# Kernel optimization log

Hardware: AMD Instinct MI355X
Metric: run time of the kernel (lower is better)

Reference implementation:

```python
import jax, jax.numpy as jnp
import numpy as np

D_MODEL = 512
NUM_HEADS = 8
DEPTH = D_MODEL // NUM_HEADS


def setup_inputs() -> dict:
    key = jax.random.key(0)
    ks = jax.random.split(key, 9)
    B, S = 2, 2048
    x = jax.random.normal(ks[0], (B, S, D_MODEL), dtype=jnp.float32)
    s = 1.0 / np.sqrt(D_MODEL)
    Wq = jax.random.uniform(ks[1], (D_MODEL, D_MODEL), minval=-s, maxval=s)
    bq = jax.random.uniform(ks[2], (D_MODEL,), minval=-s, maxval=s)
    Wk = jax.random.uniform(ks[3], (D_MODEL, D_MODEL), minval=-s, maxval=s)
    bk = jax.random.uniform(ks[4], (D_MODEL,), minval=-s, maxval=s)
    Wv = jax.random.uniform(ks[5], (D_MODEL, D_MODEL), minval=-s, maxval=s)
    bv = jax.random.uniform(ks[6], (D_MODEL,), minval=-s, maxval=s)
    Wo = jax.random.uniform(ks[7], (D_MODEL, D_MODEL), minval=-s, maxval=s)
    bo = jax.random.uniform(ks[8], (D_MODEL,), minval=-s, maxval=s)
    return {"x": x, "Wq": Wq, "bq": bq, "Wk": Wk, "bk": bk,
            "Wv": Wv, "bv": bv, "Wo": Wo, "bo": bo}


def _split_heads(t, B, S):
    # [B,S,D] -> [B,H,S,depth]
    return t.reshape(B, S, NUM_HEADS, DEPTH).transpose(0, 2, 1, 3)


def reference(x, Wq, bq, Wk, bk, Wv, bv, Wo, bo):
    B, S, _ = x.shape
    q = _split_heads(x @ Wq.T + bq, B, S) / jnp.sqrt(jnp.float32(DEPTH))
    k = _split_heads(x @ Wk.T + bk, B, S)
    v = _split_heads(x @ Wv.T + bv, B, S)
    scores = jnp.einsum('bhsd,bhtd->bhst', q, k)  # [B,H,S,S]
    attn = jax.nn.softmax(scores, axis=-1)
    out = jnp.einsum('bhst,bhtd->bhsd', attn, v)  # [B,H,S,depth]
    out = out.transpose(0, 2, 1, 3).reshape(B, S, D_MODEL)
    return out @ Wo.T + bo
```

## Files before the change

kernel.cpp:

```cpp
#include <hip/hip_runtime.h>

typedef unsigned int   uint32;
typedef unsigned short ushort16;

constexpr int BATCH = 2;
constexpr int SEQ   = 2048;
constexpr int DM    = 512;
constexpr int NH    = 8;
constexpr int DP    = 64;
constexpr int MROWS = BATCH * SEQ;
constexpr size_t HEADS_ELEMS = (size_t)BATCH * NH * SEQ * DP;

typedef short bf16x8 __attribute__((ext_vector_type(8)));
typedef float f32x4  __attribute__((ext_vector_type(4)));
typedef float f32x16 __attribute__((ext_vector_type(16)));
#define MFMA16(a, b, c) __builtin_amdgcn_mfma_f32_16x16x32_bf16((a), (b), (c), 0, 0, 0)
#define MFMA32(a, b, c) __builtin_amdgcn_mfma_f32_32x32x16_bf16((a), (b), (c), 0, 0, 0)

__device__ __forceinline__ ushort16 f2bf(float f) {
    uint32 u = __float_as_uint(f);
    uint32 r = (u + 0x7fffu + ((u >> 16) & 1u)) >> 16;
    return (ushort16)r;
}

__device__ __forceinline__ uint32 cvtpk(float a, float b) {
    uint32 r;
    asm("v_cvt_pk_bf16_f32 %0, %1, %2" : "=v"(r) : "v"(a), "v"(b));
    return r;
}

__device__ __forceinline__ bf16x8 mkfrag(uint32 u0, uint32 u1, uint32 u2, uint32 u3) {
    union { uint32 u[4]; bf16x8 v; } t;
    t.u[0] = u0; t.u[1] = u1; t.u[2] = u2; t.u[3] = u3;
    return t.v;
}

__device__ __forceinline__ void gload16(const void* g, void* l) {
    __builtin_amdgcn_global_load_lds(
        (const __attribute__((address_space(1))) unsigned int*)g,
        (__attribute__((address_space(3))) unsigned int*)l, 16, 0, 0);
}

constexpr int XF4 = (MROWS * DM) / 4;
constexpr int WF4 = (DM * DM) / 4;

__global__ __launch_bounds__(256)
void convert_inputs(const float4* __restrict__ x,  const float4* __restrict__ wq,
                    const float4* __restrict__ wk, const float4* __restrict__ wv,
                    const float4* __restrict__ wo, ushort4* __restrict__ xb,
                    ushort4* __restrict__ wqkv, ushort4* __restrict__ wob) {
    const int idx = blockIdx.x * 256 + threadIdx.x;
    float4 v; ushort4* dp;
    if (idx < XF4) { v = x[idx]; dp = xb + idx; }
    else {
        const int r = idx - XF4;
        if (r < WF4)          { v = wq[r];           dp = wqkv + r; }
        else if (r < 2 * WF4) { v = wk[r - WF4];     dp = wqkv + r; }
        else if (r < 3 * WF4) { v = wv[r - 2 * WF4]; dp = wqkv + r; }
        else                  { v = wo[r - 3 * WF4]; dp = wob + (r - 3 * WF4); }
    }
    ushort4 o = {f2bf(v.x), f2bf(v.y), f2bf(v.z), f2bf(v.w)};
    *dp = o;
}

template <int BM, int BN, int EPI, int NBX, int NBLK>
__global__ __launch_bounds__(256)
void gemm_mfma(const ushort16* __restrict__ X, const ushort16* __restrict__ Wc,
               const float* __restrict__ bq_, const float* __restrict__ bk_,
               const float* __restrict__ bv_, const float* __restrict__ bo_,
               ushort16* __restrict__ Qh, ushort16* __restrict__ Kh,
               ushort16* __restrict__ Vt, float* __restrict__ Out,
               float qscale) {
    constexpr int FM = BM / 32;
    constexpr int FN = BN / 32;
    __shared__ ushort16 As[BM * 64];
    __shared__ ushort16 Bs[BN * 64];

    const int tid  = threadIdx.x;
    const int lane = tid & 63;
    const int wid  = tid >> 6;
    const int lg   = lane >> 4;
    const int lq   = lane & 15;
    const int wr   = wid >> 1;
    const int wc   = wid & 1;

    const int bid = blockIdx.x;
    const int w   = (bid & 7) * (NBLK / 8) + (bid >> 3);
    const int bx  = w % NBX;
    const int by  = w / NBX;
    const int m0  = by * BM;
    const int n0  = bx * BN;
    const bool swapped = (EPI == 1) || (n0 < 2 * DM);

    f32x4 acc[FM][FN];
    #pragma unroll
    for (int i = 0; i < FM; i++)
        #pragma unroll
        for (int j = 0; j < FN; j++)
            #pragma unroll
            for (int r = 0; r < 4; r++) acc[i][j][r] = 0.f;

    for (int k0 = 0; k0 < DM; k0 += 64) {
        #pragma unroll
        for (int i = 0; i < BM / 32; i++) {
            const int ch = tid + i * 256;
            const int row = ch >> 3, c8 = (ch & 7) * 8;
            gload16(X + (size_t)(m0 + row) * DM + k0 + c8, As + (size_t)ch * 8);
        }
        #pragma unroll
        for (int i = 0; i < BN / 32; i++) {
            const int ch = tid + i * 256;
            const int row = ch >> 3, c8 = (ch & 7) * 8;
            gload16(Wc + (size_t)(n0 + row) * DM + k0 + c8, Bs + (size_t)ch * 8);
        }
        __syncthreads();

        bf16x8 af[FM][2], bfr[FN][2];
        #pragma unroll
        for (int i = 0; i < FM; i++)
            #pragma unroll
            for (int kk = 0; kk < 2; kk++)
                af[i][kk] = *(const bf16x8*)(As + (size_t)(wr * (BM / 2) + i * 16 + lq) * 64 + kk * 32 + lg * 8);
        #pragma unroll
        for (int j = 0; j < FN; j++)
            #pragma unroll
            for (int kk = 0; kk < 2; kk++)
                bfr[j][kk] = *(const bf16x8*)(Bs + (size_t)(wc * (BN / 2) + j * 16 + lq) * 64 + kk * 32 + lg * 8);

        if (swapped) {
            #pragma unroll
            for (int kk = 0; kk < 2; kk++)
                #pragma unroll
                for (int i = 0; i < FM; i++)
                    #pragma unroll
                    for (int j = 0; j < FN; j++)
                        acc[i][j] = MFMA16(bfr[j][kk], af[i][kk], acc[i][j]);
        } else {
            #pragma unroll
            for (int kk = 0; kk < 2; kk++)
                #pragma unroll
                for (int i = 0; i < FM; i++)
                    #pragma unroll
                    for (int j = 0; j < FN; j++)
                        acc[i][j] = MFMA16(af[i][kk], bfr[j][kk], acc[i][j]);
        }
        __syncthreads();
    }

    if (EPI == 1) {
        #pragma unroll
        for (int i = 0; i < FM; i++) {
            const int m = m0 + wr * (BM / 2) + i * 16 + lq;
            #pragma unroll
            for (int j = 0; j < FN; j++) {
                const int nr = n0 + wc * (BN / 2) + j * 16 + lg * 4;
                float4 b4 = *(const float4*)(bo_ + nr);
                float4 o;
                o.x = acc[i][j][0] + b4.x; o.y = acc[i][j][1] + b4.y;
                o.z = acc[i][j][2] + b4.z; o.w = acc[i][j][3] + b4.w;
                *(float4*)(Out + (size_t)m * DM + nr) = o;
            }
        }
    } else if (n0 < 2 * DM) {
        #pragma unroll
        for (int i = 0; i < FM; i++) {
            const int m = m0 + wr * (BM / 2) + i * 16 + lq;
            const int b = m >> 11, s = m & (SEQ - 1);
            #pragma unroll
            for (int j = 0; j < FN; j++) {
                const int nr = n0 + wc * (BN / 2) + j * 16 + lg * 4;
                const bool isq = nr < DM;
                const int rel = nr & (DM - 1);
                const int h = rel >> 6, d = rel & 63;
                float4 b4 = *(const float4*)((isq ? bq_ : bk_) + rel);
                const float sc = isq ? qscale : 1.0f;
                ushort4 o = { f2bf((acc[i][j][0] + b4.x) * sc),
                              f2bf((acc[i][j][1] + b4.y) * sc),
                              f2bf((acc[i][j][2] + b4.z) * sc),
                              f2bf((acc[i][j][3] + b4.w) * sc) };
                ushort16* dst = (isq ? Qh : Kh) +
                    (((size_t)(b * NH + h) * SEQ + s) * DP + d);
                *(ushort4*)dst = o;
            }
        }
    } else {
        #pragma unroll
        for (int j = 0; j < FN; j++) {
            const int n = n0 + wc * (BN / 2) + j * 16 + lq;
            const int rel = n - 2 * DM;
            const int h = rel >> 6, d = rel & 63;
            const float bias = bv_[rel];
            #pragma unroll
            for (int i = 0; i < FM; i++) {
                const int mr = m0 + wr * (BM / 2) + i * 16 + lg * 4;
                const int b = mr >> 11, s0 = mr & (SEQ - 1);
                ushort4 o = { f2bf(acc[i][j][0] + bias),
                              f2bf(acc[i][j][1] + bias),
                              f2bf(acc[i][j][2] + bias),
                              f2bf(acc[i][j][3] + bias) };
                ushort16* dst = Vt +
                    (((size_t)(b * NH + h) * DP + d) * SEQ + s0);
                *(ushort4*)dst = o;
            }
        }
    }
}

__global__ __launch_bounds__(1024, 1)
void attn_mfma(const ushort16* __restrict__ Q, const ushort16* __restrict__ K,
               const ushort16* __restrict__ Vt, ushort16* __restrict__ O) {
    __shared__ ushort16 Kl[3][128 * 64];
    __shared__ ushort16 Vl[3][64 * 128];
    __shared__ float    lbuf[4][4][32];

    const int tid  = threadIdx.x;
    const int lane = tid & 63;
    const int wid  = tid >> 6;
    const int qw   = wid & 3;
    const int kw   = wid >> 2;
    const int h    = lane >> 5;
    const int l31  = lane & 31;
    const int l7   = l31 & 7;

    const int bid = blockIdx.x;
    const int w   = (bid & 7) * 32 + (bid >> 3);
    const int qt  = w & 15;
    const int bh  = w >> 4;

    const int qrow = qt * 128 + qw * 32 + l31;
    const ushort16* qbase = Q + ((size_t)bh * SEQ + qrow) * DP;
    bf16x8 qf[4];
    #pragma unroll
    for (int ds = 0; ds < 4; ds++)
        qf[ds] = *(const bf16x8*)(qbase + ds * 16 + h * 8);

    f32x16 ok0, ok1;
    #pragma unroll
    for (int r = 0; r < 16; r++) { ok0[r] = 0.f; ok1[r] = 0.f; }
    float lrun = 0.f;

    const ushort16* kg = K  + (size_t)bh * SEQ * DP;
    const ushort16* vg = Vt + (size_t)bh * DP * SEQ;
    const int kr = tid >> 3, kc = tid & 7;
    const int ksrc = (kc ^ (kr & 7)) * 8;
    const ushort16* const kgp = kg + (size_t)kr * DP + ksrc;
    const int vr = tid >> 4, vc = tid & 15;
    const int vsrc = (vc ^ (vr & 7)) * 8;
    const ushort16* const vgp = vg + (size_t)vr * SEQ + vsrc;

    auto stage = [&](int buf, int t) {
        gload16(kgp + (size_t)t * 128 * DP, &Kl[buf][(size_t)tid * 8]);
        gload16(vgp + (size_t)t * 128,      &Vl[buf][(size_t)tid * 8]);
    };

    const int krow = kw * 32 + l31;
    int koff[4];
    #pragma unroll
    for (int ds = 0; ds < 4; ds++)
        koff[ds] = krow * 64 + (((ds * 2 + h) ^ l7) * 8);
    int voff[2][2];
    #pragma unroll
    for (int dt = 0; dt < 2; dt++)
        #pragma unroll
        for (int kc2 = 0; kc2 < 2; kc2++)
            voff[dt][kc2] = (dt * 32 + l31) * 128 + (((kw * 4 + kc2 * 2 + h) ^ l7) * 8);

    auto compute = [&](int buf) {
        const ushort16* kb = &Kl[buf][0];
        const ushort16* vb = &Vl[buf][0];
        f32x16 st;
        #pragma unroll
        for (int r = 0; r < 16; r++) st[r] = 0.f;
        __builtin_amdgcn_s_setprio(1);
        #pragma unroll
        for (int ds = 0; ds < 4; ds++) {
            bf16x8 kf = *(const bf16x8*)(kb + koff[ds]);
            st = MFMA32(kf, qf[ds], st);
        }
        __builtin_amdgcn_s_setprio(0);

        #pragma unroll
        for (int r = 0; r < 16; r++) {
            st[r] = __builtin_exp2f(st[r]);
            lrun += st[r];
        }

        uint32 A0 = cvtpk(st[0], st[1]),   A1 = cvtpk(st[2], st[3]);
        uint32 B0 = cvtpk(st[4], st[5]),   B1 = cvtpk(st[6], st[7]);
        uint32 C0 = cvtpk(st[8], st[9]),   C1 = cvtpk(st[10], st[11]);
        uint32 D0 = cvtpk(st[12], st[13]), D1 = cvtpk(st[14], st[15]);
        uint32 z0 = __shfl_xor((int)(h ? A0 : B0), 32);
        uint32 z1 = __shfl_xor((int)(h ? A1 : B1), 32);
        uint32 z2 = __shfl_xor((int)(h ? C0 : D0), 32);
        uint32 z3 = __shfl_xor((int)(h ? C1 : D1), 32);
        bf16x8 pa0 = h ? mkfrag(z0, z1, B0, B1) : mkfrag(A0, A1, z0, z1);
        bf16x8 pa1 = h ? mkfrag(z2, z3, D0, D1) : mkfrag(C0, C1, z2, z3);

        const bf16x8 v00 = *(const bf16x8*)(vb + voff[0][0]);
        const bf16x8 v01 = *(const bf16x8*)(vb + voff[0][1]);
        const bf16x8 v10 = *(const bf16x8*)(vb + voff[1][0]);
        const bf16x8 v11 = *(const bf16x8*)(vb + voff[1][1]);
        __builtin_amdgcn_s_setprio(1);
        ok0 = MFMA32(pa0, v00, ok0);
        ok0 = MFMA32(pa1, v01, ok0);
        ok1 = MFMA32(pa0, v10, ok1);
        ok1 = MFMA32(pa1, v11, ok1);
        __builtin_amdgcn_s_setprio(0);
    };

    #define WAITN(n) asm volatile("s_waitcnt vmcnt(" #n ")" ::: "memory")
    #define BAR() __builtin_amdgcn_s_barrier()

    stage(0, 0);
    stage(1, 1);
    int t = 0;
    #pragma unroll 1
    for (int it = 0; it < 4; ++it) {
        WAITN(2); BAR(); stage(2, t + 2); compute(0);
        WAITN(2); BAR(); stage(0, t + 3); compute(1);
        WAITN(2); BAR(); stage(1, t + 4); compute(2);
        t += 3;
    }
    WAITN(2); BAR(); stage(2, 14); compute(0);
    WAITN(2); BAR(); stage(0, 15); compute(1);
    WAITN(2); BAR(); compute(2);
    WAITN(0); BAR(); compute(0);
    #undef WAITN
    #undef BAR

    lrun += __shfl_xor(lrun, 32);

    __syncthreads();
    float* const fK = (float*)&Kl[0][0];
    float* const fV = (float*)&Vl[0][0];
    if (h == 0) lbuf[qw][kw][l31] = lrun;
    if (kw > 0) {
        const int ridx = (kw - 1) * 4 + qw;
        float* const dst = (ridx < 6) ? (fK + ridx * 2048) : (fV + (ridx - 6) * 2048);
        #pragma unroll
        for (int r = 0; r < 16; r++) {
            const int q = (r & 3) + 8 * (r >> 2) + 4 * h;
            dst[q * 64 + l31]      = ok0[r];
            dst[q * 64 + 32 + l31] = ok1[r];
        }
    }
    __syncthreads();
    if (kw == 0) {
        float* const p1 = fK + qw * 2048;
        float* const p2 = (qw < 2) ? (fK + (4 + qw) * 2048)
                                   : (fV + (qw - 2) * 2048);
        float* const p3 = fV + (2 + qw) * 2048;
        const float lsum = lbuf[qw][0][l31] + lbuf[qw][1][l31]
                         + lbuf[qw][2][l31] + lbuf[qw][3][l31];
        const float linv = 1.f / lsum;
        const int b = bh >> 3, hh = bh & 7;
        #pragma unroll
        for (int r = 0; r < 16; r++) {
            const int q = (r & 3) + 8 * (r >> 2) + 4 * h;
            const float li_q = __shfl(linv, q);
            const int o0 = q * 64 + l31;
            const int o1 = q * 64 + 32 + l31;
            const float v0 = (ok0[r] + p1[o0] + p2[o0] + p3[o0]) * li_q;
            const float v1 = (ok1[r] + p1[o1] + p2[o1] + p3[o1]) * li_q;
            const int qr = qt * 128 + qw * 32 + q;
            ushort16* orow = O + ((size_t)(b * SEQ + qr)) * DM + hh * DP;
            orow[l31]      = f2bf(v0);
            orow[32 + l31] = f2bf(v1);
        }
    }
}

extern "C" void kernel_launch(void* const* d_in, const int* in_sizes, int n_in,
                              void* d_out, int out_size, void* d_ws, size_t ws_size,
                              hipStream_t stream) {
    const float* x  = (const float*)d_in[0];
    const float* Wq = (const float*)d_in[1];
    const float* bq = (const float*)d_in[2];
    const float* Wk = (const float*)d_in[3];
    const float* bk = (const float*)d_in[4];
    const float* Wv = (const float*)d_in[5];
    const float* bv = (const float*)d_in[6];
    const float* Wo = (const float*)d_in[7];
    const float* bo = (const float*)d_in[8];
    float* out = (float*)d_out;

    ushort16* ws   = (ushort16*)d_ws;
    ushort16* xb   = ws;
    ushort16* wqkv = xb + (size_t)MROWS * DM;
    ushort16* wob  = wqkv + (size_t)3 * DM * DM;
    ushort16* qh   = wob + (size_t)DM * DM;
    ushort16* kh   = qh + HEADS_ELEMS;
    ushort16* vt   = kh + HEADS_ELEMS;
    ushort16* oh   = vt + HEADS_ELEMS;

    convert_inputs<<<dim3((XF4 + 4 * WF4) / 256), dim3(256), 0, stream>>>(
        (const float4*)x, (const float4*)Wq, (const float4*)Wk,
        (const float4*)Wv, (const float4*)Wo,
        (ushort4*)xb, (ushort4*)wqkv, (ushort4*)wob);

    const float qscale = 0.125f * 1.44269504088896f;

    gemm_mfma<128, 64, 0, 24, 768><<<dim3(768), dim3(256), 0, stream>>>(
        xb, wqkv, bq, bk, bv, bo, qh, kh, vt, nullptr, qscale);

    attn_mfma<<<dim3(256), dim3(1024), 0, stream>>>(qh, kh, vt, oh);

    gemm_mfma<64, 64, 1, 8, 512><<<dim3(512), dim3(256), 0, stream>>>(
        oh, wob, bq, bk, bv, bo, qh, kh, vt, out, qscale);
}
```

Before: 66.03 us.

## Fuse fp32-to-bf16 conversion of x into QKV GEMM and split QK accumulators

The separate pass that converts x to bf16 is removed. The QKV projection GEMM now reads fp32 x directly, packs it to bf16 with v_cvt_pk_bf16_f32 and writes it into shared memory. This saves a full write and re-read of the activation buffer but gives up async global_load_lds for the A tile, and x is now re-read once per N-tile (24 times). In the attention kernel the K and V LDS loads are hoisted to the top and the QK^T MFMA chain is split into two independent accumulators to shorten the dependency chain, at the cost of more registers.

Result: slower. 136.9 us (+107.3%).

```diff
diff --git a/kernel.cpp b/kernel.cpp
--- a/kernel.cpp
+++ b/kernel.cpp
@@ -41,31 +41,25 @@
         (__attribute__((address_space(3))) unsigned int*)l, 16, 0, 0);
 }
 
-constexpr int XF4 = (MROWS * DM) / 4;
 constexpr int WF4 = (DM * DM) / 4;
 
 __global__ __launch_bounds__(256)
-void convert_inputs(const float4* __restrict__ x,  const float4* __restrict__ wq,
-                    const float4* __restrict__ wk, const float4* __restrict__ wv,
-                    const float4* __restrict__ wo, ushort4* __restrict__ xb,
-                    ushort4* __restrict__ wqkv, ushort4* __restrict__ wob) {
-    const int idx = blockIdx.x * 256 + threadIdx.x;
+void convert_w(const float4* __restrict__ wq, const float4* __restrict__ wk,
+               const float4* __restrict__ wv, const float4* __restrict__ wo,
+               ushort4* __restrict__ wqkv, ushort4* __restrict__ wob) {
+    const int r = blockIdx.x * 256 + threadIdx.x;
     float4 v; ushort4* dp;
-    if (idx < XF4) { v = x[idx]; dp = xb + idx; }
-    else {
-        const int r = idx - XF4;
-        if (r < WF4)          { v = wq[r];           dp = wqkv + r; }
-        else if (r < 2 * WF4) { v = wk[r - WF4];     dp = wqkv + r; }
-        else if (r < 3 * WF4) { v = wv[r - 2 * WF4]; dp = wqkv + r; }
-        else                  { v = wo[r - 3 * WF4]; dp = wob + (r - 3 * WF4); }
-    }
+    if (r < WF4)          { v = wq[r];           dp = wqkv + r; }
+    else if (r < 2 * WF4) { v = wk[r - WF4];     dp = wqkv + r; }
+    else if (r < 3 * WF4) { v = wv[r - 2 * WF4]; dp = wqkv + r; }
+    else                  { v = wo[r - 3 * WF4]; dp = wob + (r - 3 * WF4); }
     ushort4 o = {f2bf(v.x), f2bf(v.y), f2bf(v.z), f2bf(v.w)};
     *dp = o;
 }
 
-template <int BM, int BN, int EPI, int NBX, int NBLK>
+template <int BM, int BN, int EPI, int NBX, int NBLK, int AFP32>
 __global__ __launch_bounds__(256)
-void gemm_mfma(const ushort16* __restrict__ X, const ushort16* __restrict__ Wc,
+void gemm_mfma(const void* __restrict__ Xv, const ushort16* __restrict__ Wc,
                const float* __restrict__ bq_, const float* __restrict__ bk_,
                const float* __restrict__ bv_, const float* __restrict__ bo_,
                ushort16* __restrict__ Qh, ushort16* __restrict__ Kh,
@@ -101,11 +95,27 @@
             for (int r = 0; r < 4; r++) acc[i][j][r] = 0.f;
 
     for (int k0 = 0; k0 < DM; k0 += 64) {
-        #pragma unroll
-        for (int i = 0; i < BM / 32; i++) {
-            const int ch = tid + i * 256;
-            const int row = ch >> 3, c8 = (ch & 7) * 8;
-            gload16(X + (size_t)(m0 + row) * DM + k0 + c8, As + (size_t)ch * 8);
+        if (AFP32) {
+            const float* Xf = (const float*)Xv;
+            #pragma unroll
+            for (int j = 0; j < BM / 16; j++) {
+                const int chunk = tid + j * 256;
+                const int row = chunk >> 4;
+                const int c4  = chunk & 15;
+                const float4 v = *(const float4*)(Xf + (size_t)(m0 + row) * DM + k0 + c4 * 4);
+                uint2 p;
+                p.x = cvtpk(v.x, v.y);
+                p.y = cvtpk(v.z, v.w);
+                *(uint2*)(As + (size_t)row * 64 + c4 * 4) = p;
+            }
+        } else {
+            const ushort16* Xb = (const ushort16*)Xv;
+            #pragma unroll
+            for (int i = 0; i < BM / 32; i++) {
+                const int ch = tid + i * 256;
+                const int row = ch >> 3, c8 = (ch & 7) * 8;
+                gload16(Xb + (size_t)(m0 + row) * DM + k0 + c8, As + (size_t)ch * 8);
+            }
         }
         #pragma unroll
         for (int i = 0; i < BN / 32; i++) {
@@ -268,22 +278,35 @@
     auto compute = [&](int buf) {
         const ushort16* kb = &Kl[buf][0];
         const ushort16* vb = &Vl[buf][0];
+        const bf16x8 kf0 = *(const bf16x8*)(kb + koff[0]);
+        const bf16x8 kf1 = *(const bf16x8*)(kb + koff[1]);
+        const bf16x8 kf2 = *(const bf16x8*)(kb + koff[2]);
+        const bf16x8 kf3 = *(const bf16x8*)(kb + koff[3]);
+        const bf16x8 v00 = *(const bf16x8*)(vb + voff[0][0]);
+        const bf16x8 v01 = *(const bf16x8*)(vb + voff[0][1]);
+        const bf16x8 v10 = *(const bf16x8*)(vb + voff[1][0]);
+        const bf16x8 v11 = *(const bf16x8*)(vb + voff[1][1]);
+
+        f32x16 sa, sb;
+        #pragma unroll
+        for (int r = 0; r < 16; r++) { sa[r] = 0.f; sb[r] = 0.f; }
+        __builtin_amdgcn_s_setprio(1);
+        sa = MFMA32(kf0, qf[0], sa);
+        sb = MFMA32(kf1, qf[1], sb);
+        sa = MFMA32(kf2, qf[2], sa);
+        sb = MFMA32(kf3, qf[3], sb);
+        __builtin_amdgcn_s_setprio(0);
+
         f32x16 st;
-        #pragma unroll
-        for (int r = 0; r < 16; r++) st[r] = 0.f;
-        __builtin_amdgcn_s_setprio(1);
-        #pragma unroll
-        for (int ds = 0; ds < 4; ds++) {
-            bf16x8 kf = *(const bf16x8*)(kb + koff[ds]);
-            st = MFMA32(kf, qf[ds], st);
-        }
-        __builtin_amdgcn_s_setprio(0);
-
-        #pragma unroll
-        for (int r = 0; r < 16; r++) {
-            st[r] = __builtin_exp2f(st[r]);
-            lrun += st[r];
-        }
+        float ps0 = 0.f, ps1 = 0.f;
+        #pragma unroll
+        for (int r = 0; r < 16; r += 2) {
+            st[r]     = __builtin_exp2f(sa[r] + sb[r]);
+            st[r + 1] = __builtin_exp2f(sa[r + 1] + sb[r + 1]);
+            ps0 += st[r];
+            ps1 += st[r + 1];
+        }
+        lrun += ps0 + ps1;
 
         uint32 A0 = cvtpk(st[0], st[1]),   A1 = cvtpk(st[2], st[3]);
         uint32 B0 = cvtpk(st[4], st[5]),   B1 = cvtpk(st[6], st[7]);
@@ -296,10 +319,6 @@
         bf16x8 pa0 = h ? mkfrag(z0, z1, B0, B1) : mkfrag(A0, A1, z0, z1);
         bf16x8 pa1 = h ? mkfrag(z2, z3, D0, D1) : mkfrag(C0, C1, z2, z3);
 
-        const bf16x8 v00 = *(const bf16x8*)(vb + voff[0][0]);
-        const bf16x8 v01 = *(const bf16x8*)(vb + voff[0][1]);
-        const bf16x8 v10 = *(const bf16x8*)(vb + voff[1][0]);
-        const bf16x8 v11 = *(const bf16x8*)(vb + voff[1][1]);
         __builtin_amdgcn_s_setprio(1);
         ok0 = MFMA32(pa0, v00, ok0);
         ok0 = MFMA32(pa1, v01, ok0);
@@ -393,18 +412,17 @@
     ushort16* vt   = kh + HEADS_ELEMS;
     ushort16* oh   = vt + HEADS_ELEMS;
 
-    convert_inputs<<<dim3((XF4 + 4 * WF4) / 256), dim3(256), 0, stream>>>(
-        (const float4*)x, (const float4*)Wq, (const float4*)Wk,
-        (const float4*)Wv, (const float4*)Wo,
-        (ushort4*)xb, (ushort4*)wqkv, (ushort4*)wob);
+    convert_w<<<dim3((4 * WF4) / 256), dim3(256), 0, stream>>>(
+        (const float4*)Wq, (const float4*)Wk, (const float4*)Wv,
+        (const float4*)Wo, (ushort4*)wqkv, (ushort4*)wob);
 
     const float qscale = 0.125f * 1.44269504088896f;
 
-    gemm_mfma<128, 64, 0, 24, 768><<<dim3(768), dim3(256), 0, stream>>>(
-        xb, wqkv, bq, bk, bv, bo, qh, kh, vt, nullptr, qscale);
+    gemm_mfma<128, 64, 0, 24, 768, 1><<<dim3(768), dim3(256), 0, stream>>>(
+        x, wqkv, bq, bk, bv, bo, qh, kh, vt, nullptr, qscale);
 
     attn_mfma<<<dim3(256), dim3(1024), 0, stream>>>(qh, kh, vt, oh);
 
-    gemm_mfma<64, 64, 1, 8, 512><<<dim3(512), dim3(256), 0, stream>>>(
+    gemm_mfma<64, 64, 1, 8, 512, 0><<<dim3(512), dim3(256), 0, stream>>>(
         oh, wob, bq, bk, bv, bo, qh, kh, vt, out, qscale);
 }
```

## Double-buffer 256-key tiles instead of triple-buffering 128-key tiles in attention

Applied to the files above, without the earlier changes.

Switches the attention K/V staging from three LDS buffers of 128 keys to two buffers of 256 keys. This halves the number of barrier-separated pipeline steps, and each warp now processes two 32-key row groups per step. The cost is an extra barrier before each refill, so the loop no longer overlaps a load into a third buffer with compute. The cross-warp reduction scratch layout is remapped to fit the new LDS buffer sizes.

Result: no change. 65.91 us (-0.2%).

```diff
diff --git a/kernel.cpp b/kernel.cpp
--- a/kernel.cpp
+++ b/kernel.cpp
@@ -209,8 +209,8 @@
 __global__ __launch_bounds__(1024, 1)
 void attn_mfma(const ushort16* __restrict__ Q, const ushort16* __restrict__ K,
                const ushort16* __restrict__ Vt, ushort16* __restrict__ O) {
-    __shared__ ushort16 Kl[3][128 * 64];
-    __shared__ ushort16 Vl[3][64 * 128];
+    __shared__ ushort16 Kl[2][256 * 64];
+    __shared__ ushort16 Vl[2][64 * 256];
     __shared__ float    lbuf[4][4][32];
 
     const int tid  = threadIdx.x;
@@ -243,69 +243,84 @@
     const ushort16* vg = Vt + (size_t)bh * DP * SEQ;
     const int kr = tid >> 3, kc = tid & 7;
     const int ksrc = (kc ^ (kr & 7)) * 8;
-    const ushort16* const kgp = kg + (size_t)kr * DP + ksrc;
-    const int vr = tid >> 4, vc = tid & 15;
+    const ushort16* const kgp0 = kg + (size_t)kr * DP + ksrc;
+    const ushort16* const kgp1 = kg + (size_t)(kr + 128) * DP + ksrc;
+    const int vr = tid >> 5, vc = tid & 31;
     const int vsrc = (vc ^ (vr & 7)) * 8;
-    const ushort16* const vgp = vg + (size_t)vr * SEQ + vsrc;
+    const ushort16* const vgp0 = vg + (size_t)vr * SEQ + vsrc;
+    const ushort16* const vgp1 = vg + (size_t)(vr + 32) * SEQ + vsrc;
 
     auto stage = [&](int buf, int t) {
-        gload16(kgp + (size_t)t * 128 * DP, &Kl[buf][(size_t)tid * 8]);
-        gload16(vgp + (size_t)t * 128,      &Vl[buf][(size_t)tid * 8]);
+        const size_t ko = (size_t)t * 256 * DP;
+        const size_t vo = (size_t)t * 256;
+        gload16(kgp0 + ko, &Kl[buf][(size_t)tid * 8]);
+        gload16(kgp1 + ko, &Kl[buf][(size_t)(tid + 1024) * 8]);
+        gload16(vgp0 + vo, &Vl[buf][(size_t)tid * 8]);
+        gload16(vgp1 + vo, &Vl[buf][(size_t)(tid + 1024) * 8]);
     };
 
-    const int krow = kw * 32 + l31;
-    int koff[4];
+    int koff[2][4];
     #pragma unroll
-    for (int ds = 0; ds < 4; ds++)
-        koff[ds] = krow * 64 + (((ds * 2 + h) ^ l7) * 8);
-    int voff[2][2];
+    for (int rg = 0; rg < 2; rg++) {
+        const int krow = kw * 64 + rg * 32 + l31;
+        #pragma unroll
+        for (int ds = 0; ds < 4; ds++)
+            koff[rg][ds] = krow * 64 + (((ds * 2 + h) ^ l7) * 8);
+    }
+    int voff[2][2][2];
     #pragma unroll
     for (int dt = 0; dt < 2; dt++)
         #pragma unroll
-        for (int kc2 = 0; kc2 < 2; kc2++)
-            voff[dt][kc2] = (dt * 32 + l31) * 128 + (((kw * 4 + kc2 * 2 + h) ^ l7) * 8);
+        for (int rg = 0; rg < 2; rg++)
+            #pragma unroll
+            for (int kc2 = 0; kc2 < 2; kc2++)
+                voff[dt][rg][kc2] = (dt * 32 + l31) * 256 +
+                    (((kw * 8 + rg * 4 + kc2 * 2 + h) ^ l7) * 8);
 
     auto compute = [&](int buf) {
         const ushort16* kb = &Kl[buf][0];
         const ushort16* vb = &Vl[buf][0];
-        f32x16 st;
-        #pragma unroll
-        for (int r = 0; r < 16; r++) st[r] = 0.f;
-        __builtin_amdgcn_s_setprio(1);
-        #pragma unroll
-        for (int ds = 0; ds < 4; ds++) {
-            bf16x8 kf = *(const bf16x8*)(kb + koff[ds]);
-            st = MFMA32(kf, qf[ds], st);
-        }
-        __builtin_amdgcn_s_setprio(0);
-
-        #pragma unroll
-        for (int r = 0; r < 16; r++) {
-            st[r] = __builtin_exp2f(st[r]);
-            lrun += st[r];
-        }
-
-        uint32 A0 = cvtpk(st[0], st[1]),   A1 = cvtpk(st[2], st[3]);
-        uint32 B0 = cvtpk(st[4], st[5]),   B1 = cvtpk(st[6], st[7]);
-        uint32 C0 = cvtpk(st[8], st[9]),   C1 = cvtpk(st[10], st[11]);
-        uint32 D0 = cvtpk(st[12], st[13]), D1 = cvtpk(st[14], st[15]);
-        uint32 z0 = __shfl_xor((int)(h ? A0 : B0), 32);
-        uint32 z1 = __shfl_xor((int)(h ? A1 : B1), 32);
-        uint32 z2 = __shfl_xor((int)(h ? C0 : D0), 32);
-        uint32 z3 = __shfl_xor((int)(h ? C1 : D1), 32);
-        bf16x8 pa0 = h ? mkfrag(z0, z1, B0, B1) : mkfrag(A0, A1, z0, z1);
-        bf16x8 pa1 = h ? mkfrag(z2, z3, D0, D1) : mkfrag(C0, C1, z2, z3);
-
-        const bf16x8 v00 = *(const bf16x8*)(vb + voff[0][0]);
-        const bf16x8 v01 = *(const bf16x8*)(vb + voff[0][1]);
-        const bf16x8 v10 = *(const bf16x8*)(vb + voff[1][0]);
-        const bf16x8 v11 = *(const bf16x8*)(vb + voff[1][1]);
-        __builtin_amdgcn_s_setprio(1);
-        ok0 = MFMA32(pa0, v00, ok0);
-        ok0 = MFMA32(pa1, v01, ok0);
-        ok1 = MFMA32(pa0, v10, ok1);
-        ok1 = MFMA32(pa1, v11, ok1);
-        __builtin_amdgcn_s_setprio(0);
+        #pragma unroll
+        for (int rg = 0; rg < 2; rg++) {
+            f32x16 st;
+            #pragma unroll
+            for (int r = 0; r < 16; r++) st[r] = 0.f;
+            __builtin_amdgcn_s_setprio(1);
+            #pragma unroll
+            for (int ds = 0; ds < 4; ds++) {
+                bf16x8 kf = *(const bf16x8*)(kb + koff[rg][ds]);
+                st = MFMA32(kf, qf[ds], st);
+            }
+            __builtin_amdgcn_s_setprio(0);
+
+            #pragma unroll
+            for (int r = 0; r < 16; r++) {
+                st[r] = __builtin_exp2f(st[r]);
+                lrun += st[r];
+            }
+
+            uint32 A0 = cvtpk(st[0], st[1]),   A1 = cvtpk(st[2], st[3]);
+            uint32 B0 = cvtpk(st[4], st[5]),   B1 = cvtpk(st[6], st[7]);
+            uint32 C0 = cvtpk(st[8], st[9]),   C1 = cvtpk(st[10], st[11]);
+            uint32 D0 = cvtpk(st[12], st[13]), D1 = cvtpk(st[14], st[15]);
+            uint32 z0 = __shfl_xor((int)(h ? A0 : B0), 32);
+            uint32 z1 = __shfl_xor((int)(h ? A1 : B1), 32);
+            uint32 z2 = __shfl_xor((int)(h ? C0 : D0), 32);
+            uint32 z3 = __shfl_xor((int)(h ? C1 : D1), 32);
+            bf16x8 pa0 = h ? mkfrag(z0, z1, B0, B1) : mkfrag(A0, A1, z0, z1);
+            bf16x8 pa1 = h ? mkfrag(z2, z3, D0, D1) : mkfrag(C0, C1, z2, z3);
+
+            const bf16x8 v00 = *(const bf16x8*)(vb + voff[0][rg][0]);
+            const bf16x8 v01 = *(const bf16x8*)(vb + voff[0][rg][1]);
+            const bf16x8 v10 = *(const bf16x8*)(vb + voff[1][rg][0]);
+            const bf16x8 v11 = *(const bf16x8*)(vb + voff[1][rg][1]);
+            __builtin_amdgcn_s_setprio(1);
+            ok0 = MFMA32(pa0, v00, ok0);
+            ok0 = MFMA32(pa1, v01, ok0);
+            ok1 = MFMA32(pa0, v10, ok1);
+            ok1 = MFMA32(pa1, v11, ok1);
+            __builtin_amdgcn_s_setprio(0);
+        }
     };
 
     #define WAITN(n) asm volatile("s_waitcnt vmcnt(" #n ")" ::: "memory")
@@ -313,18 +328,15 @@
 
     stage(0, 0);
     stage(1, 1);
-    int t = 0;
     #pragma unroll 1
-    for (int it = 0; it < 4; ++it) {
-        WAITN(2); BAR(); stage(2, t + 2); compute(0);
-        WAITN(2); BAR(); stage(0, t + 3); compute(1);
-        WAITN(2); BAR(); stage(1, t + 4); compute(2);
-        t += 3;
-    }
-    WAITN(2); BAR(); stage(2, 14); compute(0);
-    WAITN(2); BAR(); stage(0, 15); compute(1);
-    WAITN(2); BAR(); compute(2);
-    WAITN(0); BAR(); compute(0);
+    for (int t = 0; t < 7; ++t) {
+        WAITN(4); BAR();
+        compute(t & 1);
+        BAR();
+        if (t < 6) stage(t & 1, t + 2);
+    }
+    WAITN(0); BAR();
+    compute(1);
     #undef WAITN
     #undef BAR
 
@@ -336,7 +348,7 @@
     if (h == 0) lbuf[qw][kw][l31] = lrun;
     if (kw > 0) {
         const int ridx = (kw - 1) * 4 + qw;
-        float* const dst = (ridx < 6) ? (fK + ridx * 2048) : (fV + (ridx - 6) * 2048);
+        float* const dst = (ridx < 8) ? (fK + ridx * 2048) : (fV + (ridx - 8) * 2048);
         #pragma unroll
         for (int r = 0; r < 16; r++) {
             const int q = (r & 3) + 8 * (r >> 2) + 4 * h;
@@ -347,9 +359,8 @@
     __syncthreads();
     if (kw == 0) {
         float* const p1 = fK + qw * 2048;
-        float* const p2 = (qw < 2) ? (fK + (4 + qw) * 2048)
-                                   : (fV + (qw - 2) * 2048);
-        float* const p3 = fV + (2 + qw) * 2048;
+        float* const p2 = fK + (4 + qw) * 2048;
+        float* const p3 = fV + qw * 2048;
         const float lsum = lbuf[qw][0][l31] + lbuf[qw][1][l31]
                          + lbuf[qw][2][l31] + lbuf[qw][3][l31];
         const float linv = 1.f / lsum;
```
